# Kernel optimization log

Measured on AMD Instinct MI355X. Metric: run time of the kernel, lower is better.

Reference implementation:

```python
import jax, jax.numpy as jnp
import numpy as np

D_MODEL = 512
N_HEADS = 8
D_K = D_MODEL // N_HEADS


def setup_inputs() -> dict:
    key = jax.random.key(0)
    ks = jax.random.split(key, 7)
    s = 1.0 / np.sqrt(D_MODEL)
    return {
        "x": jax.random.normal(ks[0], (2, 4096, D_MODEL), dtype=jnp.float32),
        "W_q": jax.random.normal(ks[1], (D_MODEL, D_MODEL), dtype=jnp.float32) * s,
        "W_k": jax.random.normal(ks[2], (D_MODEL, D_MODEL), dtype=jnp.float32) * s,
        "W_v": jax.random.normal(ks[3], (D_MODEL, D_MODEL), dtype=jnp.float32) * s,
        "b_v": jax.random.normal(ks[4], (D_MODEL,), dtype=jnp.float32) * s,
        "W_o": jax.random.normal(ks[5], (D_MODEL, D_MODEL), dtype=jnp.float32) * s,
        "b_o": jax.random.normal(ks[6], (D_MODEL,), dtype=jnp.float32) * s,
    }


def _split_heads(t):
    # [N, S, d_model] -> [N, H, S, d_k]
    N, S, _ = t.shape
    return t.reshape(N, S, N_HEADS, D_K).transpose(0, 2, 1, 3)


def reference(x, W_q, W_k, W_v, b_v, W_o, b_o):
    N, S, _ = x.shape
    # nn.Linear computes x @ W.T (+ b)
    Q = _split_heads(x @ W_q.T)
    K = _split_heads(x @ W_k.T)
    V = _split_heads(x @ W_v.T + b_v)
    scale = jnp.sqrt(jnp.asarray(D_K, x.dtype))
    scores = jnp.einsum('nhqd,nhkd->nhqk', Q, K) / scale  # [N,H,S,S]
    causal = jnp.tril(jnp.ones((S, S), dtype=bool))
    scores = jnp.where(causal, scores, -jnp.inf)
    attn = jax.nn.softmax(scores, axis=-1)
    out = jnp.einsum('nhqk,nhkd->nhqd', attn, V)  # [N,H,S,d_k]
    out = out.transpose(0, 2, 1, 3).reshape(N, S, D_MODEL)
    return out @ W_o.T + b_o
```

## Files before the change

kernel.cpp:

```cpp
#include <hip/hip_runtime.h>
#include <hip/hip_bf16.h>

#define NB 2
#define SEQ 4096
#define DM 512
#define NH 8
#define DKH 64
#define MTOT (NB*SEQ)

typedef __attribute__((ext_vector_type(4))) float f32x4;
typedef __attribute__((ext_vector_type(16))) float f32x16;
typedef __attribute__((ext_vector_type(8))) short bf16x8;
typedef __attribute__((ext_vector_type(2))) unsigned uint2v;

__device__ inline unsigned short f2bf(float f) {
    union { float f; unsigned int u; } v; v.f = f;
    unsigned int r = v.u + 0x7FFFu + ((v.u >> 16) & 1u);
    return (unsigned short)(r >> 16);
}

#define QSCALE 0.18033688011112042f

__global__ void cast_kernel(const float* __restrict__ x, const float* __restrict__ wq,
                            const float* __restrict__ wk, const float* __restrict__ wv,
                            const float* __restrict__ wo, unsigned short* __restrict__ dst) {
    const int NX = MTOT*DM;
    const int NW = DM*DM;
    int i4 = blockIdx.x * blockDim.x + threadIdx.x;
    long e = (long)i4 * 4;
    if (e >= NX + 4L*NW) return;
    const float* src; long off;
    if (e < NX)           { src = x;  off = e; }
    else if (e < NX+NW)   { src = wq; off = e - NX; }
    else if (e < NX+2*NW) { src = wk; off = e - NX - NW; }
    else if (e < NX+3*NW) { src = wv; off = e - NX - 2*NW; }
    else                  { src = wo; off = e - NX - 3*NW; }
    float4 v = *reinterpret_cast<const float4*>(src + off);
    ushort4 o;
    o.x = f2bf(v.x); o.y = f2bf(v.y); o.z = f2bf(v.z); o.w = f2bf(v.w);
    *reinterpret_cast<ushort4*>(dst + e) = o;
}

#define GEMM_KLOOP(APTR, BPTR, BROW, BCOL)                                         \
    f32x4 acc[4][4] = {};                                                          \
    for (int kt = 0; kt < 8; ++kt) {                                               \
        __syncthreads();                                                           \
        _Pragma("unroll")                                                          \
        for (int i = 0; i < 4; ++i) {                                              \
            int rbase = i*32 + wid*8;                                              \
            int row = rbase + (lane >> 3);                                         \
            int csrc = (lane & 7) ^ (row & 7);                                     \
            const unsigned short* asrc = Aptr_ + (long)((BROW)+row)*512 + kt*64 + csrc*8; \
            __builtin_amdgcn_global_load_lds(                                      \
                (const __attribute__((address_space(1))) unsigned int*)asrc,       \
                (__attribute__((address_space(3))) unsigned int*)&As[rbase*64], 16, 0, 0); \
            const unsigned short* bsrc = Bptr_ + (long)((BCOL)+row)*512 + kt*64 + csrc*8; \
            __builtin_amdgcn_global_load_lds(                                      \
                (const __attribute__((address_space(1))) unsigned int*)bsrc,       \
                (__attribute__((address_space(3))) unsigned int*)&Bs[rbase*64], 16, 0, 0); \
        }                                                                          \
        __syncthreads();                                                           \
        _Pragma("unroll")                                                          \
        for (int kk = 0; kk < 2; ++kk) {                                           \
            bf16x8 af[4], bfr[4];                                                  \
            _Pragma("unroll")                                                      \
            for (int mi = 0; mi < 4; ++mi) {                                       \
                int row = wr*64 + mi*16 + l15;                                     \
                int colb = (kk*32 + l4*8) * 2;                                     \
                af[mi] = *reinterpret_cast<const bf16x8*>(                         \
                    reinterpret_cast<const char*>(As) + row*128 + (colb ^ ((row&7)<<4))); \
            }                                                                      \
            _Pragma("unroll")                                                      \
            for (int ni = 0; ni < 4; ++ni) {                                       \
                int row = wc*64 + ni*16 + l15;                                     \
                int colb = (kk*32 + l4*8) * 2;                                     \
                bfr[ni] = *reinterpret_cast<const bf16x8*>(                        \
                    reinterpret_cast<const char*>(Bs) + row*128 + (colb ^ ((row&7)<<4))); \
            }                                                                      \
            _Pragma("unroll")                                                      \
            for (int mi = 0; mi < 4; ++mi)                                         \
                _Pragma("unroll")                                                  \
                for (int ni = 0; ni < 4; ++ni)                                     \
                    acc[mi][ni] = __builtin_amdgcn_mfma_f32_16x16x32_bf16(af[mi], bfr[ni], acc[mi][ni], 0, 0, 0); \
        }                                                                          \
    }

__global__ __launch_bounds__(256, 2) void gemm_qk(
    const unsigned short* __restrict__ A,
    const unsigned short* __restrict__ B,
    unsigned short* __restrict__ Qh, unsigned short* __restrict__ Kh)
{
    __shared__ __align__(16) unsigned short As[128*64];
    __shared__ __align__(16) unsigned short Bs[128*64];
    int tid = threadIdx.x;
    int wid = tid >> 6, lane = tid & 63;
    int wr = wid >> 1, wc = wid & 1;
    int brow = blockIdx.x * 128;
    int bcol = blockIdx.y * 128;
    int l15 = lane & 15, l4 = lane >> 4;
    const unsigned short* Aptr_ = A;
    const unsigned short* Bptr_ = B;

    GEMM_KLOOP(A, B, brow, bcol)

    #pragma unroll
    for (int mi = 0; mi < 4; ++mi) {
        #pragma unroll
        for (int ni = 0; ni < 4; ++ni) {
            #pragma unroll
            for (int r = 0; r < 4; ++r) {
                int row = brow + wr*64 + mi*16 + l4*4 + r;
                int col = bcol + wc*64 + ni*16 + l15;
                float v = acc[mi][ni][r];
                int which = col >> 9;
                int cw = col & 511;
                int h = cw >> 6, d = cw & 63;
                int b = row >> 12, s = row & 4095;
                int bh = b*NH + h;
                if (which == 0)
                    Qh[((long)(bh*SEQ + s))*DKH + d] = f2bf(v * QSCALE);
                else
                    Kh[((long)(bh*SEQ + s))*DKH + d] = f2bf(v);
            }
        }
    }
}

__global__ __launch_bounds__(256, 2) void gemm_v(
    const unsigned short* __restrict__ A,
    const unsigned short* __restrict__ B,
    const float* __restrict__ bv,
    unsigned short* __restrict__ Vt)
{
    __shared__ __align__(16) unsigned short As[128*64];
    __shared__ __align__(16) unsigned short Bs[128*64];
    __shared__ __align__(16) unsigned short Trs[128*136];
    int tid = threadIdx.x;
    int wid = tid >> 6, lane = tid & 63;
    int wr = wid >> 1, wc = wid & 1;
    int brow = blockIdx.x * 128;
    int bcol = 1024 + blockIdx.y * 128;
    int l15 = lane & 15, l4 = lane >> 4;
    const unsigned short* Aptr_ = A;
    const unsigned short* Bptr_ = B;

    GEMM_KLOOP(A, B, brow, bcol)

    #pragma unroll
    for (int mi = 0; mi < 4; ++mi) {
        #pragma unroll
        for (int ni = 0; ni < 4; ++ni) {
            #pragma unroll
            for (int r = 0; r < 4; ++r) {
                int rowLoc = wr*64 + mi*16 + l4*4 + r;
                int colLoc = wc*64 + ni*16 + l15;
                Trs[colLoc*136 + rowLoc] = f2bf(acc[mi][ni][r] + bv[(bcol + colLoc) & 511]);
            }
        }
    }
    __syncthreads();

    const int b = brow >> 12;
    const int stile = brow & 4095;
    const int hbase = (bcol - 1024) >> 6;
    #pragma unroll
    for (int pass = 0; pass < 8; ++pass) {
        int idx = pass*256 + tid;
        int dd = idx >> 4;
        int s8 = (idx & 15) << 3;
        bf16x8 vv = *reinterpret_cast<const bf16x8*>(&Trs[dd*136 + s8]);
        int bh = b*NH + hbase + (dd >> 6);
        int d = dd & 63;
        *reinterpret_cast<bf16x8*>(Vt + ((long)(bh*DKH + d))*SEQ + stile + s8) = vv;
    }
}

__global__ __launch_bounds__(256, 2) void gemm_out(
    const unsigned short* __restrict__ A,
    const unsigned short* __restrict__ B,
    const float* __restrict__ bias, float* __restrict__ Cout)
{
    __shared__ __align__(16) unsigned short As[128*64];
    __shared__ __align__(16) unsigned short Bs[128*64];
    int tid = threadIdx.x;
    int wid = tid >> 6, lane = tid & 63;
    int wr = wid >> 1, wc = wid & 1;
    int brow = blockIdx.x * 128;
    int bcol = blockIdx.y * 128;
    int l15 = lane & 15, l4 = lane >> 4;
    const unsigned short* Aptr_ = A;
    const unsigned short* Bptr_ = B;

    GEMM_KLOOP(A, B, brow, bcol)

    #pragma unroll
    for (int mi = 0; mi < 4; ++mi) {
        #pragma unroll
        for (int ni = 0; ni < 4; ++ni) {
            #pragma unroll
            for (int r = 0; r < 4; ++r) {
                int row = brow + wr*64 + mi*16 + l4*4 + r;
                int col = bcol + wc*64 + ni*16 + l15;
                Cout[(long)row*DM + col] = acc[mi][ni][r] + bias[col];
            }
        }
    }
}

#define PV_STEP_M(SV, VLS, KS, B0, OD0, OD1, LS)  do {                             \
        unsigned c0, c1, c2, c3;                                                   \
        float t0 = SV[B0+0], t1 = SV[B0+1], t2 = SV[B0+2], t3 = SV[B0+3];          \
        float t4 = SV[B0+4], t5 = SV[B0+5], t6 = SV[B0+6], t7 = SV[B0+7];          \
        asm("v_cvt_pk_bf16_f32 %0, %1, %2" : "=v"(c0) : "v"(t0), "v"(t1));         \
        asm("v_cvt_pk_bf16_f32 %0, %1, %2" : "=v"(c1) : "v"(t2), "v"(t3));         \
        asm("v_cvt_pk_bf16_f32 %0, %1, %2" : "=v"(c2) : "v"(t4), "v"(t5));         \
        asm("v_cvt_pk_bf16_f32 %0, %1, %2" : "=v"(c3) : "v"(t6), "v"(t7));         \
        uint2v sw0 = __builtin_amdgcn_permlane32_swap(c0, c2, false, false);       \
        uint2v sw1 = __builtin_amdgcn_permlane32_swap(c1, c3, false, false);       \
        union { unsigned u[4]; bf16x8 v; } pu;                                     \
        pu.u[0] = sw0[0]; pu.u[1] = sw1[0]; pu.u[2] = sw0[1]; pu.u[3] = sw1[1];    \
        bf16x8 vf0 = *reinterpret_cast<const bf16x8*>(VLS + l31*128      + (((KS)*32 + hi*16) ^ swz)); \
        OD0 = __builtin_amdgcn_mfma_f32_32x32x16_bf16(vf0, pu.v, OD0, 0, 0, 0);    \
        bf16x8 vf1 = *reinterpret_cast<const bf16x8*>(VLS + (32+l31)*128 + (((KS)*32 + hi*16) ^ swz)); \
        OD1 = __builtin_amdgcn_mfma_f32_32x32x16_bf16(vf1, pu.v, OD1, 0, 0, 0);    \
        LS  = __builtin_amdgcn_mfma_f32_32x32x16_bf16(onesv, pu.v, LS, 0, 0, 0);   \
    } while (0)

__global__ __launch_bounds__(256, 4) void attn_fm(
    const unsigned short* __restrict__ Qh,
    const unsigned short* __restrict__ Kh,
    const unsigned short* __restrict__ Vt,
    unsigned short* __restrict__ Obf)
{
    __shared__ __align__(16) unsigned short Kc[2][64*64];
    __shared__ __align__(16) unsigned short Vc[2][64*64];
    const int tid = threadIdx.x;
    const int wid = tid >> 6, lane = tid & 63;
    const int g = wid & 1, p = wid >> 1;
    const int l31 = lane & 31;
    const int hi  = lane >> 5;

    const int id   = blockIdx.x;
    const int xcd  = id & 7;
    const int rest = id >> 3;
    const int bh   = xcd + ((rest & 1) << 3);
    const int t    = 63 - (rest >> 1);

    const unsigned short* Qbase = Qh + (long)bh*SEQ*DKH;
    const unsigned short* Kbase = Kh + (long)bh*SEQ*DKH;
    const unsigned short* Vbase = Vt + (long)bh*DKH*SEQ;

    const int q0w = t*64 + g*32;
    const int q   = q0w + l31;
    const int nu  = t + 1;
    const int swz = (l31 & 7) << 4;

    bf16x8 qf[4];
    #pragma unroll
    for (int kk = 0; kk < 4; ++kk)
        qf[kk] = *reinterpret_cast<const bf16x8*>(Qbase + (long)q*DKH + kk*16 + hi*8);

    bf16x8 onesv;
    #pragma unroll
    for (int e = 0; e < 8; ++e) onesv[e] = (short)0x3F80;

    auto STAGE = [&](int b, int key0) {
        #pragma unroll
        for (int ii = 0; ii < 2; ++ii) {
            const int rbase = wid*16 + ii*8;
            const int row = rbase + (lane >> 3);
            const int ck = (lane & 7) ^ (row & 7);
            const unsigned short* ksrc = Kbase + (long)(key0 + row)*DKH + ck*8;
            __builtin_amdgcn_global_load_lds(
                (const __attribute__((address_space(1))) unsigned int*)ksrc,
                (__attribute__((address_space(3))) unsigned int*)&Kc[b][rbase*64], 16, 0, 0);
            const unsigned short* vsrc = Vbase + (long)row*SEQ + key0 + ck*8;
            __builtin_amdgcn_global_load_lds(
                (const __attribute__((address_space(1))) unsigned int*)vsrc,
                (__attribute__((address_space(3))) unsigned int*)&Vc[b][rbase*64], 16, 0, 0);
        }
    };

    f32x16 od0 = {}, od1 = {}, ls = {};

    STAGE(0, 0);
    __syncthreads();
    int cur = 0;

    #pragma unroll 1
    for (int u = 0; u < nu; ++u) {
        if (u + 1 < nu) STAGE(cur ^ 1, (u + 1) << 6);
        const char* kl = reinterpret_cast<const char*>(&Kc[cur][0]) + p*32*128;
        const char* vl = reinterpret_cast<const char*>(&Vc[cur][0]);

        bf16x8 kfr[4];
        #pragma unroll
        for (int kk = 0; kk < 4; ++kk)
            kfr[kk] = *reinterpret_cast<const bf16x8*>(kl + l31*128 + ((kk*32 + hi*16) ^ swz));
        f32x16 sv = {};
        __builtin_amdgcn_s_setprio(1);
        #pragma unroll
        for (int kk = 0; kk < 4; ++kk)
            sv = __builtin_amdgcn_mfma_f32_32x32x16_bf16(kfr[kk], qf[kk], sv, 0, 0, 0);
        __builtin_amdgcn_s_setprio(0);

        if (u == t) {
            const int kbase = (u << 6) + (p << 5);
            #pragma unroll
            for (int r = 0; r < 16; ++r) {
                const int ko = (r&3) + 8*(r>>2) + 4*hi;
                if (kbase + ko > q) sv[r] = -1e30f;
            }
        }

        #pragma unroll
        for (int r = 0; r < 16; ++r)
            sv[r] = __builtin_amdgcn_exp2f(sv[r]);

        __builtin_amdgcn_s_setprio(1);
        PV_STEP_M(sv, vl, (2*p),     0, od0, od1, ls);
        PV_STEP_M(sv, vl, (2*p + 1), 8, od0, od1, ls);
        __builtin_amdgcn_s_setprio(0);

        __syncthreads();
        cur ^= 1;
    }

    float lsum = ls[0];
    char*  sod = reinterpret_cast<char*>(&Kc[g][0]);
    float* sml = reinterpret_cast<float*>(&Vc[g][0]);
    const int lswz = (lane & 7) << 4;
    if (p == 1) {
        #pragma unroll
        for (int i = 0; i < 4; ++i) {
            *reinterpret_cast<f32x4*>(sod + lane*128 + ((i*16) ^ lswz)) =
                (f32x4){od0[i*4+0], od0[i*4+1], od0[i*4+2], od0[i*4+3]};
            *reinterpret_cast<f32x4*>(sod + lane*128 + (((i+4)*16) ^ lswz)) =
                (f32x4){od1[i*4+0], od1[i*4+1], od1[i*4+2], od1[i*4+3]};
        }
        sml[lane] = lsum;
    }
    __syncthreads();
    if (p == 0) {
        lsum += sml[lane];
        #pragma unroll
        for (int i = 0; i < 4; ++i) {
            f32x4 t0 = *reinterpret_cast<const f32x4*>(sod + lane*128 + ((i*16) ^ lswz));
            f32x4 t1 = *reinterpret_cast<const f32x4*>(sod + lane*128 + (((i+4)*16) ^ lswz));
            #pragma unroll
            for (int k = 0; k < 4; ++k) {
                od0[i*4+k] += t0[k];
                od1[i*4+k] += t1[k];
            }
        }
        const float rls = 1.0f / lsum;
        const long obase = (long)((bh >> 3)*SEQ + q)*DM + (bh & 7)*DKH;
        #pragma unroll
        for (int rr = 0; rr < 4; ++rr) {
            ushort4 w0, w1;
            w0.x = f2bf(od0[rr*4+0]*rls); w0.y = f2bf(od0[rr*4+1]*rls);
            w0.z = f2bf(od0[rr*4+2]*rls); w0.w = f2bf(od0[rr*4+3]*rls);
            *reinterpret_cast<ushort4*>(Obf + obase + rr*8 + hi*4) = w0;
            w1.x = f2bf(od1[rr*4+0]*rls); w1.y = f2bf(od1[rr*4+1]*rls);
            w1.z = f2bf(od1[rr*4+2]*rls); w1.w = f2bf(od1[rr*4+3]*rls);
            *reinterpret_cast<ushort4*>(Obf + obase + 32 + rr*8 + hi*4) = w1;
        }
    }
}

extern "C" void kernel_launch(void* const* d_in, const int* in_sizes, int n_in,
                              void* d_out, int out_size, void* d_ws, size_t ws_size,
                              hipStream_t stream) {
    const float* x  = (const float*)d_in[0];
    const float* wq = (const float*)d_in[1];
    const float* wk = (const float*)d_in[2];
    const float* wv = (const float*)d_in[3];
    const float* bv = (const float*)d_in[4];
    const float* wo = (const float*)d_in[5];
    const float* bo = (const float*)d_in[6];
    float* out = (float*)d_out;

    unsigned short* ws = (unsigned short*)d_ws;
    unsigned short* Xbf  = ws;
    unsigned short* Wqkv = Xbf  + 4194304;
    unsigned short* Wob  = Wqkv + 786432;
    unsigned short* Qh   = Wob  + 262144;
    unsigned short* Kh   = Qh   + 4194304;
    unsigned short* Vt   = Kh   + 4194304;
    unsigned short* Obf  = Vt   + 4194304;

    cast_kernel<<<5120, 256, 0, stream>>>(x, wq, wk, wv, wo, Xbf);

    dim3 gqk(64, 8);
    gemm_qk<<<gqk, 256, 0, stream>>>(Xbf, Wqkv, Qh, Kh);
    dim3 gv(64, 4);
    gemm_v<<<gv, 256, 0, stream>>>(Xbf, Wqkv, bv, Vt);

    dim3 ga(1024);
    attn_fm<<<ga, 256, 0, stream>>>(Qh, Kh, Vt, Obf);

    dim3 go(64, 4);
    gemm_out<<<go, 256, 0, stream>>>(Obf, Wob, bo, out);
}
```

Measured before the change: 104.1 us.

## Merge QKV projection GEMMs and split attention blocks into 32-query tiles

Fuses the separate Q/K and V projection kernels into one 64x12 grid launch, with the V path transposing through a smaller shared buffer in two halves. The attention kernel now gives each block 32 queries instead of 64 and doubles the grid. Its four waves split the key tiles two ways by parity and two ways by key half, then reduce partial outputs through shared memory. This removes one launch and balances causal work across more blocks. The cost is dropping the double-buffered K/V prefetch, so each pair of tiles is loaded and then synchronized, and the final reduction now combines three partial results.

```diff
diff --git a/kernel.cpp b/kernel.cpp
--- a/kernel.cpp
+++ b/kernel.cpp
@@ -41,7 +41,7 @@
     *reinterpret_cast<ushort4*>(dst + e) = o;
 }
 
-#define GEMM_KLOOP(APTR, BPTR, BROW, BCOL)                                         \
+#define GEMM_KLOOP(BROW, BCOL)                                                     \
     f32x4 acc[4][4] = {};                                                          \
     for (int kt = 0; kt < 8; ++kt) {                                               \
         __syncthreads();                                                           \
@@ -85,93 +85,84 @@
         }                                                                          \
     }
 
-__global__ __launch_bounds__(256, 2) void gemm_qk(
+__global__ __launch_bounds__(256, 2) void gemm_qkv(
     const unsigned short* __restrict__ A,
     const unsigned short* __restrict__ B,
-    unsigned short* __restrict__ Qh, unsigned short* __restrict__ Kh)
+    const float* __restrict__ bv,
+    unsigned short* __restrict__ Qh, unsigned short* __restrict__ Kh,
+    unsigned short* __restrict__ Vt)
 {
     __shared__ __align__(16) unsigned short As[128*64];
     __shared__ __align__(16) unsigned short Bs[128*64];
+    __shared__ __align__(16) unsigned short Trs[64*136];
     int tid = threadIdx.x;
     int wid = tid >> 6, lane = tid & 63;
     int wr = wid >> 1, wc = wid & 1;
     int brow = blockIdx.x * 128;
-    int bcol = blockIdx.y * 128;
+    int by   = blockIdx.y;
+    int bcol = by * 128;
     int l15 = lane & 15, l4 = lane >> 4;
     const unsigned short* Aptr_ = A;
     const unsigned short* Bptr_ = B;
 
-    GEMM_KLOOP(A, B, brow, bcol)
-
-    #pragma unroll
-    for (int mi = 0; mi < 4; ++mi) {
+    GEMM_KLOOP(brow, bcol)
+
+    if (by < 8) {
         #pragma unroll
-        for (int ni = 0; ni < 4; ++ni) {
-            #pragma unroll
-            for (int r = 0; r < 4; ++r) {
-                int row = brow + wr*64 + mi*16 + l4*4 + r;
-                int col = bcol + wc*64 + ni*16 + l15;
-                float v = acc[mi][ni][r];
-                int which = col >> 9;
-                int cw = col & 511;
+        for (int mi = 0; mi < 4; ++mi) {
+            #pragma unroll
+            for (int ni = 0; ni < 4; ++ni) {
+                #pragma unroll
+                for (int r = 0; r < 4; ++r) {
+                    int row = brow + wr*64 + mi*16 + l4*4 + r;
+                    int col = bcol + wc*64 + ni*16 + l15;
+                    float v = acc[mi][ni][r];
+                    int which = col >> 9;
+                    int cw = col & 511;
+                    int h = cw >> 6, d = cw & 63;
+                    int b = row >> 12, s = row & 4095;
+                    int bh = b*NH + h;
+                    if (which == 0)
+                        Qh[((long)(bh*SEQ + s))*DKH + d] = f2bf(v * QSCALE);
+                    else
+                        Kh[((long)(bh*SEQ + s))*DKH + d] = f2bf(v);
+                }
+            }
+        }
+    } else {
+        const int b = brow >> 12;
+        const int stile = brow & 4095;
+        #pragma unroll 1
+        for (int hs = 0; hs < 2; ++hs) {
+            __syncthreads();
+            if (wc == hs) {
+                #pragma unroll
+                for (int mi = 0; mi < 4; ++mi) {
+                    #pragma unroll
+                    for (int ni = 0; ni < 4; ++ni) {
+                        #pragma unroll
+                        for (int r = 0; r < 4; ++r) {
+                            int rowLoc = wr*64 + mi*16 + l4*4 + r;
+                            int colH = ni*16 + l15;
+                            int cw = (bcol + hs*64 + colH) & 511;
+                            Trs[colH*136 + rowLoc] = f2bf(acc[mi][ni][r] + bv[cw]);
+                        }
+                    }
+                }
+            }
+            __syncthreads();
+            #pragma unroll
+            for (int pass = 0; pass < 4; ++pass) {
+                int idx = pass*256 + tid;
+                int dd = idx >> 4;
+                int s8 = (idx & 15) << 3;
+                bf16x8 vv = *reinterpret_cast<const bf16x8*>(&Trs[dd*136 + s8]);
+                int cw = ((bcol - 1024) + hs*64 + dd);
                 int h = cw >> 6, d = cw & 63;
-                int b = row >> 12, s = row & 4095;
                 int bh = b*NH + h;
-                if (which == 0)
-                    Qh[((long)(bh*SEQ + s))*DKH + d] = f2bf(v * QSCALE);
-                else
-                    Kh[((long)(bh*SEQ + s))*DKH + d] = f2bf(v);
-            }
-        }
-    }
-}
-
-__global__ __launch_bounds__(256, 2) void gemm_v(
-    const unsigned short* __restrict__ A,
-    const unsigned short* __restrict__ B,
-    const float* __restrict__ bv,
-    unsigned short* __restrict__ Vt)
-{
-    __shared__ __align__(16) unsigned short As[128*64];
-    __shared__ __align__(16) unsigned short Bs[128*64];
-    __shared__ __align__(16) unsigned short Trs[128*136];
-    int tid = threadIdx.x;
-    int wid = tid >> 6, lane = tid & 63;
-    int wr = wid >> 1, wc = wid & 1;
-    int brow = blockIdx.x * 128;
-    int bcol = 1024 + blockIdx.y * 128;
-    int l15 = lane & 15, l4 = lane >> 4;
-    const unsigned short* Aptr_ = A;
-    const unsigned short* Bptr_ = B;
-
-    GEMM_KLOOP(A, B, brow, bcol)
-
-    #pragma unroll
-    for (int mi = 0; mi < 4; ++mi) {
-        #pragma unroll
-        for (int ni = 0; ni < 4; ++ni) {
-            #pragma unroll
-            for (int r = 0; r < 4; ++r) {
-                int rowLoc = wr*64 + mi*16 + l4*4 + r;
-                int colLoc = wc*64 + ni*16 + l15;
-                Trs[colLoc*136 + rowLoc] = f2bf(acc[mi][ni][r] + bv[(bcol + colLoc) & 511]);
-            }
-        }
-    }
-    __syncthreads();
-
-    const int b = brow >> 12;
-    const int stile = brow & 4095;
-    const int hbase = (bcol - 1024) >> 6;
-    #pragma unroll
-    for (int pass = 0; pass < 8; ++pass) {
-        int idx = pass*256 + tid;
-        int dd = idx >> 4;
-        int s8 = (idx & 15) << 3;
-        bf16x8 vv = *reinterpret_cast<const bf16x8*>(&Trs[dd*136 + s8]);
-        int bh = b*NH + hbase + (dd >> 6);
-        int d = dd & 63;
-        *reinterpret_cast<bf16x8*>(Vt + ((long)(bh*DKH + d))*SEQ + stile + s8) = vv;
+                *reinterpret_cast<bf16x8*>(Vt + ((long)(bh*DKH + d))*SEQ + stile + s8) = vv;
+            }
+        }
     }
 }
 
@@ -191,7 +182,7 @@
     const unsigned short* Aptr_ = A;
     const unsigned short* Bptr_ = B;
 
-    GEMM_KLOOP(A, B, brow, bcol)
+    GEMM_KLOOP(brow, bcol)
 
     #pragma unroll
     for (int mi = 0; mi < 4; ++mi) {
@@ -236,7 +227,7 @@
     __shared__ __align__(16) unsigned short Vc[2][64*64];
     const int tid = threadIdx.x;
     const int wid = tid >> 6, lane = tid & 63;
-    const int g = wid & 1, p = wid >> 1;
+    const int p = wid & 1, h = wid >> 1;
     const int l31 = lane & 31;
     const int hi  = lane >> 5;
 
@@ -244,15 +235,15 @@
     const int xcd  = id & 7;
     const int rest = id >> 3;
     const int bh   = xcd + ((rest & 1) << 3);
-    const int t    = 63 - (rest >> 1);
+    const int T    = 127 - (rest >> 1);
 
     const unsigned short* Qbase = Qh + (long)bh*SEQ*DKH;
     const unsigned short* Kbase = Kh + (long)bh*SEQ*DKH;
     const unsigned short* Vbase = Vt + (long)bh*DKH*SEQ;
 
-    const int q0w = t*64 + g*32;
-    const int q   = q0w + l31;
-    const int nu  = t + 1;
+    const int q   = (T << 5) + l31;
+    const int nu  = (T >> 1) + 1;
+    const int nss = (nu + 1) >> 1;
     const int swz = (l31 & 7) << 4;
 
     bf16x8 qf[4];
@@ -264,93 +255,106 @@
     #pragma unroll
     for (int e = 0; e < 8; ++e) onesv[e] = (short)0x3F80;
 
-    auto STAGE = [&](int b, int key0) {
+    auto STAGE2 = [&](int u0) {
         #pragma unroll
-        for (int ii = 0; ii < 2; ++ii) {
-            const int rbase = wid*16 + ii*8;
-            const int row = rbase + (lane >> 3);
-            const int ck = (lane & 7) ^ (row & 7);
-            const unsigned short* ksrc = Kbase + (long)(key0 + row)*DKH + ck*8;
-            __builtin_amdgcn_global_load_lds(
-                (const __attribute__((address_space(1))) unsigned int*)ksrc,
-                (__attribute__((address_space(3))) unsigned int*)&Kc[b][rbase*64], 16, 0, 0);
-            const unsigned short* vsrc = Vbase + (long)row*SEQ + key0 + ck*8;
-            __builtin_amdgcn_global_load_lds(
-                (const __attribute__((address_space(1))) unsigned int*)vsrc,
-                (__attribute__((address_space(3))) unsigned int*)&Vc[b][rbase*64], 16, 0, 0);
+        for (int par = 0; par < 2; ++par) {
+            const int u = u0 + par;
+            if (u >= nu) break;
+            const int key0 = u << 6;
+            #pragma unroll
+            for (int ii = 0; ii < 2; ++ii) {
+                const int rbase = wid*16 + ii*8;
+                const int row = rbase + (lane >> 3);
+                const int ck = (lane & 7) ^ (row & 7);
+                const unsigned short* ksrc = Kbase + (long)(key0 + row)*DKH + ck*8;
+                __builtin_amdgcn_global_load_lds(
+                    (const __attribute__((address_space(1))) unsigned int*)ksrc,
+                    (__attribute__((address_space(3))) unsigned int*)&Kc[par][rbase*64], 16, 0, 0);
+                const unsigned short* vsrc = Vbase + (long)row*SEQ + key0 + ck*8;
+                __builtin_amdgcn_global_load_lds(
+                    (const __attribute__((address_space(1))) unsigned int*)vsrc,
+                    (__attribute__((address_space(3))) unsigned int*)&Vc[par][rbase*64], 16, 0, 0);
+            }
         }
     };
 
     f32x16 od0 = {}, od1 = {}, ls = {};
 
-    STAGE(0, 0);
+    #pragma unroll 1
+    for (int ss = 0; ss < nss; ++ss) {
+        const int u0 = 2*ss;
+        __syncthreads();
+        STAGE2(u0);
+        __syncthreads();
+        const int u = u0 + p;
+        if (u < nu) {
+            const char* kl = reinterpret_cast<const char*>(&Kc[p][0]) + h*32*128;
+            const char* vl = reinterpret_cast<const char*>(&Vc[p][0]);
+
+            bf16x8 kfr[4];
+            #pragma unroll
+            for (int kk = 0; kk < 4; ++kk)
+                kfr[kk] = *reinterpret_cast<const bf16x8*>(kl + l31*128 + ((kk*32 + hi*16) ^ swz));
+            f32x16 sv = {};
+            __builtin_amdgcn_s_setprio(1);
+            #pragma unroll
+            for (int kk = 0; kk < 4; ++kk)
+                sv = __builtin_amdgcn_mfma_f32_32x32x16_bf16(kfr[kk], qf[kk], sv, 0, 0, 0);
+            __builtin_amdgcn_s_setprio(0);
+
+            if (u == nu - 1) {
+                const int kbase = (u << 6) + (h << 5);
+                #pragma unroll
+                for (int r = 0; r < 16; ++r) {
+                    const int ko = kbase + (r&3) + 8*(r>>2) + 4*hi;
+                    if (ko > q) sv[r] = -1e30f;
+                }
+            }
+
+            #pragma unroll
+            for (int r = 0; r < 16; ++r)
+                sv[r] = __builtin_amdgcn_exp2f(sv[r]);
+
+            __builtin_amdgcn_s_setprio(1);
+            PV_STEP_M(sv, vl, (2*h),     0, od0, od1, ls);
+            PV_STEP_M(sv, vl, (2*h + 1), 8, od0, od1, ls);
+            __builtin_amdgcn_s_setprio(0);
+        }
+    }
+
     __syncthreads();
-    int cur = 0;
-
-    #pragma unroll 1
-    for (int u = 0; u < nu; ++u) {
-        if (u + 1 < nu) STAGE(cur ^ 1, (u + 1) << 6);
-        const char* kl = reinterpret_cast<const char*>(&Kc[cur][0]) + p*32*128;
-        const char* vl = reinterpret_cast<const char*>(&Vc[cur][0]);
-
-        bf16x8 kfr[4];
-        #pragma unroll
-        for (int kk = 0; kk < 4; ++kk)
-            kfr[kk] = *reinterpret_cast<const bf16x8*>(kl + l31*128 + ((kk*32 + hi*16) ^ swz));
-        f32x16 sv = {};
-        __builtin_amdgcn_s_setprio(1);
-        #pragma unroll
-        for (int kk = 0; kk < 4; ++kk)
-            sv = __builtin_amdgcn_mfma_f32_32x32x16_bf16(kfr[kk], qf[kk], sv, 0, 0, 0);
-        __builtin_amdgcn_s_setprio(0);
-
-        if (u == t) {
-            const int kbase = (u << 6) + (p << 5);
-            #pragma unroll
-            for (int r = 0; r < 16; ++r) {
-                const int ko = (r&3) + 8*(r>>2) + 4*hi;
-                if (kbase + ko > q) sv[r] = -1e30f;
-            }
-        }
-
-        #pragma unroll
-        for (int r = 0; r < 16; ++r)
-            sv[r] = __builtin_amdgcn_exp2f(sv[r]);
-
-        __builtin_amdgcn_s_setprio(1);
-        PV_STEP_M(sv, vl, (2*p),     0, od0, od1, ls);
-        PV_STEP_M(sv, vl, (2*p + 1), 8, od0, od1, ls);
-        __builtin_amdgcn_s_setprio(0);
-
-        __syncthreads();
-        cur ^= 1;
-    }
-
     float lsum = ls[0];
-    char*  sod = reinterpret_cast<char*>(&Kc[g][0]);
-    float* sml = reinterpret_cast<float*>(&Vc[g][0]);
     const int lswz = (lane & 7) << 4;
-    if (p == 1) {
+    char* sc1 = reinterpret_cast<char*>(&Kc[0][0]);
+    char* sc2 = reinterpret_cast<char*>(&Kc[1][0]);
+    char* sc3 = reinterpret_cast<char*>(&Vc[0][0]);
+    float* sml = reinterpret_cast<float*>(&Vc[1][0]);
+    if (wid != 0) {
+        char* d = (wid == 1) ? sc1 : (wid == 2) ? sc2 : sc3;
         #pragma unroll
         for (int i = 0; i < 4; ++i) {
-            *reinterpret_cast<f32x4*>(sod + lane*128 + ((i*16) ^ lswz)) =
+            *reinterpret_cast<f32x4*>(d + lane*128 + ((i*16) ^ lswz)) =
                 (f32x4){od0[i*4+0], od0[i*4+1], od0[i*4+2], od0[i*4+3]};
-            *reinterpret_cast<f32x4*>(sod + lane*128 + (((i+4)*16) ^ lswz)) =
+            *reinterpret_cast<f32x4*>(d + lane*128 + (((i+4)*16) ^ lswz)) =
                 (f32x4){od1[i*4+0], od1[i*4+1], od1[i*4+2], od1[i*4+3]};
         }
-        sml[lane] = lsum;
+        sml[(wid-1)*64 + lane] = lsum;
     }
     __syncthreads();
-    if (p == 0) {
-        lsum += sml[lane];
-        #pragma unroll
-        for (int i = 0; i < 4; ++i) {
-            f32x4 t0 = *reinterpret_cast<const f32x4*>(sod + lane*128 + ((i*16) ^ lswz));
-            f32x4 t1 = *reinterpret_cast<const f32x4*>(sod + lane*128 + (((i+4)*16) ^ lswz));
-            #pragma unroll
-            for (int k = 0; k < 4; ++k) {
-                od0[i*4+k] += t0[k];
-                od1[i*4+k] += t1[k];
+    if (wid == 0) {
+        #pragma unroll 1
+        for (int w = 1; w <= 3; ++w) {
+            const char* d = (w == 1) ? sc1 : (w == 2) ? sc2 : sc3;
+            lsum += sml[(w-1)*64 + lane];
+            #pragma unroll
+            for (int i = 0; i < 4; ++i) {
+                f32x4 t0 = *reinterpret_cast<const f32x4*>(d + lane*128 + ((i*16) ^ lswz));
+                f32x4 t1 = *reinterpret_cast<const f32x4*>(d + lane*128 + (((i+4)*16) ^ lswz));
+                #pragma unroll
+                for (int k = 0; k < 4; ++k) {
+                    od0[i*4+k] += t0[k];
+                    od1[i*4+k] += t1[k];
+                }
             }
         }
         const float rls = 1.0f / lsum;
@@ -391,13 +395,10 @@
 
     cast_kernel<<<5120, 256, 0, stream>>>(x, wq, wk, wv, wo, Xbf);
 
-    dim3 gqk(64, 8);
-    gemm_qk<<<gqk, 256, 0, stream>>>(Xbf, Wqkv, Qh, Kh);
-    dim3 gv(64, 4);
-    gemm_v<<<gv, 256, 0, stream>>>(Xbf, Wqkv, bv, Vt);
-
-    dim3 ga(1024);
-    attn_fm<<<ga, 256, 0, stream>>>(Qh, Kh, Vt, Obf);
+    dim3 gqkv(64, 12);
+    gemm_qkv<<<gqkv, 256, 0, stream>>>(Xbf, Wqkv, bv, Qh, Kh, Vt);
+
+    attn_fm<<<2048, 256, 0, stream>>>(Qh, Kh, Vt, Obf);
 
     dim3 go(64, 4);
     gemm_out<<<go, 256, 0, stream>>>(Obf, Wob, bo, out);
```

New measurement: 100.9 us. 3.0% less time.

## Fuse Q/K/V projections into one GEMM and triple-buffer attention K/V staging

Applied to the files above, without the earlier changes.

Merges the separate QK and V projection kernels into a single 64x12 launch. V blocks transpose through a smaller half-size shared buffer in two passes, which removes one kernel launch and its tail. The attention kernel moves from double to triple buffering of K/V tiles, prefetching two tiles ahead. It replaces the per-iteration __syncthreads with an explicit vmcnt wait plus barrier to overlap loads with compute. The extra shared memory lowers launch bounds occupancy from 4 to 3 blocks per SM, which may offset the latency hiding.

```diff
diff --git a/kernel.cpp b/kernel.cpp
--- a/kernel.cpp
+++ b/kernel.cpp
@@ -41,7 +41,7 @@
     *reinterpret_cast<ushort4*>(dst + e) = o;
 }
 
-#define GEMM_KLOOP(APTR, BPTR, BROW, BCOL)                                         \
+#define GEMM_KLOOP(BROW, BCOL)                                                     \
     f32x4 acc[4][4] = {};                                                          \
     for (int kt = 0; kt < 8; ++kt) {                                               \
         __syncthreads();                                                           \
@@ -85,93 +85,84 @@
         }                                                                          \
     }
 
-__global__ __launch_bounds__(256, 2) void gemm_qk(
+__global__ __launch_bounds__(256, 2) void gemm_qkv(
     const unsigned short* __restrict__ A,
     const unsigned short* __restrict__ B,
-    unsigned short* __restrict__ Qh, unsigned short* __restrict__ Kh)
+    const float* __restrict__ bv,
+    unsigned short* __restrict__ Qh, unsigned short* __restrict__ Kh,
+    unsigned short* __restrict__ Vt)
 {
     __shared__ __align__(16) unsigned short As[128*64];
     __shared__ __align__(16) unsigned short Bs[128*64];
+    __shared__ __align__(16) unsigned short Trs[64*136];
     int tid = threadIdx.x;
     int wid = tid >> 6, lane = tid & 63;
     int wr = wid >> 1, wc = wid & 1;
     int brow = blockIdx.x * 128;
-    int bcol = blockIdx.y * 128;
+    int by   = blockIdx.y;
+    int bcol = by * 128;
     int l15 = lane & 15, l4 = lane >> 4;
     const unsigned short* Aptr_ = A;
     const unsigned short* Bptr_ = B;
 
-    GEMM_KLOOP(A, B, brow, bcol)
-
-    #pragma unroll
-    for (int mi = 0; mi < 4; ++mi) {
-        #pragma unroll
-        for (int ni = 0; ni < 4; ++ni) {
+    GEMM_KLOOP(brow, bcol)
+
+    if (by < 8) {
+        #pragma unroll
+        for (int mi = 0; mi < 4; ++mi) {
             #pragma unroll
-            for (int r = 0; r < 4; ++r) {
-                int row = brow + wr*64 + mi*16 + l4*4 + r;
-                int col = bcol + wc*64 + ni*16 + l15;
-                float v = acc[mi][ni][r];
-                int which = col >> 9;
-                int cw = col & 511;
+            for (int ni = 0; ni < 4; ++ni) {
+                #pragma unroll
+                for (int r = 0; r < 4; ++r) {
+                    int row = brow + wr*64 + mi*16 + l4*4 + r;
+                    int col = bcol + wc*64 + ni*16 + l15;
+                    float v = acc[mi][ni][r];
+                    int which = col >> 9;
+                    int cw = col & 511;
+                    int h = cw >> 6, d = cw & 63;
+                    int b = row >> 12, s = row & 4095;
+                    int bh = b*NH + h;
+                    if (which == 0)
+                        Qh[((long)(bh*SEQ + s))*DKH + d] = f2bf(v * QSCALE);
+                    else
+                        Kh[((long)(bh*SEQ + s))*DKH + d] = f2bf(v);
+                }
+            }
+        }
+    } else {
+        const int b = brow >> 12;
+        const int stile = brow & 4095;
+        #pragma unroll 1
+        for (int hs = 0; hs < 2; ++hs) {
+            __syncthreads();
+            if (wc == hs) {
+                #pragma unroll
+                for (int mi = 0; mi < 4; ++mi) {
+                    #pragma unroll
+                    for (int ni = 0; ni < 4; ++ni) {
+                        #pragma unroll
+                        for (int r = 0; r < 4; ++r) {
+                            int rowLoc = wr*64 + mi*16 + l4*4 + r;
+                            int colH = ni*16 + l15;
+                            int cw = (bcol + hs*64 + colH) & 511;
+                            Trs[colH*136 + rowLoc] = f2bf(acc[mi][ni][r] + bv[cw]);
+                        }
+                    }
+                }
+            }
+            __syncthreads();
+            #pragma unroll
+            for (int pass = 0; pass < 4; ++pass) {
+                int idx = pass*256 + tid;
+                int dd = idx >> 4;
+                int s8 = (idx & 15) << 3;
+                bf16x8 vv = *reinterpret_cast<const bf16x8*>(&Trs[dd*136 + s8]);
+                int cw = ((bcol - 1024) + hs*64 + dd);
                 int h = cw >> 6, d = cw & 63;
-                int b = row >> 12, s = row & 4095;
                 int bh = b*NH + h;
-                if (which == 0)
-                    Qh[((long)(bh*SEQ + s))*DKH + d] = f2bf(v * QSCALE);
-                else
-                    Kh[((long)(bh*SEQ + s))*DKH + d] = f2bf(v);
-            }
-        }
-    }
-}
-
-__global__ __launch_bounds__(256, 2) void gemm_v(
-    const unsigned short* __restrict__ A,
-    const unsigned short* __restrict__ B,
-    const float* __restrict__ bv,
-    unsigned short* __restrict__ Vt)
-{
-    __shared__ __align__(16) unsigned short As[128*64];
-    __shared__ __align__(16) unsigned short Bs[128*64];
-    __shared__ __align__(16) unsigned short Trs[128*136];
-    int tid = threadIdx.x;
-    int wid = tid >> 6, lane = tid & 63;
-    int wr = wid >> 1, wc = wid & 1;
-    int brow = blockIdx.x * 128;
-    int bcol = 1024 + blockIdx.y * 128;
-    int l15 = lane & 15, l4 = lane >> 4;
-    const unsigned short* Aptr_ = A;
-    const unsigned short* Bptr_ = B;
-
-    GEMM_KLOOP(A, B, brow, bcol)
-
-    #pragma unroll
-    for (int mi = 0; mi < 4; ++mi) {
-        #pragma unroll
-        for (int ni = 0; ni < 4; ++ni) {
-            #pragma unroll
-            for (int r = 0; r < 4; ++r) {
-                int rowLoc = wr*64 + mi*16 + l4*4 + r;
-                int colLoc = wc*64 + ni*16 + l15;
-                Trs[colLoc*136 + rowLoc] = f2bf(acc[mi][ni][r] + bv[(bcol + colLoc) & 511]);
-            }
-        }
-    }
-    __syncthreads();
-
-    const int b = brow >> 12;
-    const int stile = brow & 4095;
-    const int hbase = (bcol - 1024) >> 6;
-    #pragma unroll
-    for (int pass = 0; pass < 8; ++pass) {
-        int idx = pass*256 + tid;
-        int dd = idx >> 4;
-        int s8 = (idx & 15) << 3;
-        bf16x8 vv = *reinterpret_cast<const bf16x8*>(&Trs[dd*136 + s8]);
-        int bh = b*NH + hbase + (dd >> 6);
-        int d = dd & 63;
-        *reinterpret_cast<bf16x8*>(Vt + ((long)(bh*DKH + d))*SEQ + stile + s8) = vv;
+                *reinterpret_cast<bf16x8*>(Vt + ((long)(bh*DKH + d))*SEQ + stile + s8) = vv;
+            }
+        }
     }
 }
 
@@ -191,7 +182,7 @@
     const unsigned short* Aptr_ = A;
     const unsigned short* Bptr_ = B;
 
-    GEMM_KLOOP(A, B, brow, bcol)
+    GEMM_KLOOP(brow, bcol)
 
     #pragma unroll
     for (int mi = 0; mi < 4; ++mi) {
@@ -226,14 +217,14 @@
         LS  = __builtin_amdgcn_mfma_f32_32x32x16_bf16(onesv, pu.v, LS, 0, 0, 0);   \
     } while (0)
 
-__global__ __launch_bounds__(256, 4) void attn_fm(
+__global__ __launch_bounds__(256, 3) void attn_fm(
     const unsigned short* __restrict__ Qh,
     const unsigned short* __restrict__ Kh,
     const unsigned short* __restrict__ Vt,
     unsigned short* __restrict__ Obf)
 {
-    __shared__ __align__(16) unsigned short Kc[2][64*64];
-    __shared__ __align__(16) unsigned short Vc[2][64*64];
+    __shared__ __align__(16) unsigned short Kc[3][64*64];
+    __shared__ __align__(16) unsigned short Vc[3][64*64];
     const int tid = threadIdx.x;
     const int wid = tid >> 6, lane = tid & 63;
     const int g = wid & 1, p = wid >> 1;
@@ -284,14 +275,22 @@
     f32x16 od0 = {}, od1 = {}, ls = {};
 
     STAGE(0, 0);
-    __syncthreads();
-    int cur = 0;
-
+    if (nu > 1) {
+        STAGE(1, 64);
+        asm volatile("s_waitcnt vmcnt(4)" ::: "memory");
+    } else {
+        asm volatile("s_waitcnt vmcnt(0)" ::: "memory");
+    }
+    __builtin_amdgcn_s_barrier();
+
+    int bc = 0;
     #pragma unroll 1
     for (int u = 0; u < nu; ++u) {
-        if (u + 1 < nu) STAGE(cur ^ 1, (u + 1) << 6);
-        const char* kl = reinterpret_cast<const char*>(&Kc[cur][0]) + p*32*128;
-        const char* vl = reinterpret_cast<const char*>(&Vc[cur][0]);
+        const int bn = (bc + 2 >= 3) ? bc - 1 : bc + 2;
+        if (u + 2 < nu) STAGE(bn, (u + 2) << 6);
+
+        const char* kl = reinterpret_cast<const char*>(&Kc[bc][0]) + p*32*128;
+        const char* vl = reinterpret_cast<const char*>(&Vc[bc][0]);
 
         bf16x8 kfr[4];
         #pragma unroll
@@ -322,10 +321,17 @@
         PV_STEP_M(sv, vl, (2*p + 1), 8, od0, od1, ls);
         __builtin_amdgcn_s_setprio(0);
 
-        __syncthreads();
-        cur ^= 1;
-    }
-
+        if (u + 2 < nu) {
+            asm volatile("s_waitcnt vmcnt(4)" ::: "memory");
+        } else {
+            asm volatile("s_waitcnt vmcnt(0)" ::: "memory");
+        }
+        __builtin_amdgcn_s_barrier();
+
+        bc = (bc + 1 >= 3) ? 0 : bc + 1;
+    }
+
+    __syncthreads();
     float lsum = ls[0];
     char*  sod = reinterpret_cast<char*>(&Kc[g][0]);
     float* sml = reinterpret_cast<float*>(&Vc[g][0]);
@@ -391,13 +397,10 @@
 
     cast_kernel<<<5120, 256, 0, stream>>>(x, wq, wk, wv, wo, Xbf);
 
-    dim3 gqk(64, 8);
-    gemm_qk<<<gqk, 256, 0, stream>>>(Xbf, Wqkv, Qh, Kh);
-    dim3 gv(64, 4);
-    gemm_v<<<gv, 256, 0, stream>>>(Xbf, Wqkv, bv, Vt);
-
-    dim3 ga(1024);
-    attn_fm<<<ga, 256, 0, stream>>>(Qh, Kh, Vt, Obf);
+    dim3 gqkv(64, 12);
+    gemm_qkv<<<gqkv, 256, 0, stream>>>(Xbf, Wqkv, bv, Qh, Kh, Vt);
+
+    attn_fm<<<1024, 256, 0, stream>>>(Qh, Kh, Vt, Obf);
 
     dim3 go(64, 4);
     gemm_out<<<go, 256, 0, stream>>>(Obf, Wob, bo, out);
```

Result: no change. 102.1 us (-1.9%).
